# Kernel tuning notes

Hardware: AMD Instinct MI355X
Metric: run time of the kernel (lower is better)

The kernel has to match this reference:

```python
import jax, jax.numpy as jnp
import numpy as np

B = 8192
D = 512          # hidden_dim
OBS_EMB = 256
COMM = 128
N_ACT = 4
N_LAYERS = 2
D_INNER = 2 * D
D_STATE = 16
DT_RANK = D // 16  # 32
D_CONV = 4
EPS = 1e-5


def _xavier(k, shape):
    s = jnp.sqrt(2.0 / (shape[-2] + shape[-1]))
    return jax.random.normal(k, shape, jnp.float32) * s


def setup_inputs() -> dict:
    ks = jax.random.split(jax.random.key(0), 16)
    p = {}
    p['obs'] = jax.random.normal(ks[0], (B, 75), jnp.float32)
    p['comm_in'] = jax.random.normal(ks[1], (B, COMM), jnp.float32)
    # obs encoder: Conv2d(3->32, k=3, valid) + Linear(288->256)
    p['conv_w'] = jax.random.normal(ks[2], (32, 3, 3, 3), jnp.float32) * jnp.sqrt(2.0 / 27.0)
    p['conv_b'] = jnp.zeros((32,), jnp.float32)
    p['enc_w'] = _xavier(ks[3], (288, OBS_EMB))
    p['enc_b'] = jnp.zeros((OBS_EMB,), jnp.float32)
    p['proj_w'] = _xavier(ks[4], (OBS_EMB + COMM, D))
    p['proj_b'] = jnp.zeros((D,), jnp.float32)
    # Mamba stack params (stacked over layers)
    p['norm_w'] = jnp.ones((N_LAYERS, D), jnp.float32)
    p['in_proj_w'] = _xavier(ks[5], (N_LAYERS, D, 2 * D_INNER))
    p['conv1d_w'] = jax.random.normal(ks[6], (N_LAYERS, D_INNER, D_CONV), jnp.float32) / jnp.sqrt(D_CONV)
    p['conv1d_b'] = jnp.zeros((N_LAYERS, D_INNER), jnp.float32)
    p['x_proj_w'] = _xavier(ks[7], (N_LAYERS, D_INNER, DT_RANK + 2 * D_STATE))
    p['dt_proj_w'] = _xavier(ks[8], (N_LAYERS, DT_RANK, D_INNER))
    p['dt_proj_b'] = jnp.full((N_LAYERS, D_INNER), jnp.log(jnp.expm1(0.01)), jnp.float32)  # dt ~ 0.01
    p['A_log'] = jnp.log(jnp.broadcast_to(jnp.arange(1, D_STATE + 1, dtype=jnp.float32), (N_LAYERS, D_INNER, D_STATE)))
    p['D_param'] = jnp.ones((N_LAYERS, D_INNER), jnp.float32)
    p['out_proj_w'] = _xavier(ks[9], (N_LAYERS, D_INNER, D))
    p['final_norm_w'] = jnp.ones((D,), jnp.float32)
    # output heads
    p['act_w'] = _xavier(ks[10], (D, N_ACT)); p['act_b'] = jnp.zeros((N_ACT,), jnp.float32)
    p['comm_w'] = _xavier(ks[11], (D, COMM)); p['comm_b'] = jnp.zeros((COMM,), jnp.float32)
    p['val_w'] = _xavier(ks[12], (D, 1)); p['val_b'] = jnp.zeros((1,), jnp.float32)
    return p


def _rmsnorm(x, w):
    return x * jax.lax.rsqrt(jnp.mean(x * x, axis=-1, keepdims=True) + EPS) * w


def _mamba_block(u, Wi, cw, cb, Wx, Wdt, bdt, Alog, Dp, Wo):
    # u: (B, L, D) -> (B, L, D)
    Bsz, L, _ = u.shape
    d_inner = Dp.shape[0]
    x, z = jnp.split(u @ Wi, 2, axis=-1)                       # (B,L,di) each
    # causal depthwise conv1d over L
    xt = jnp.pad(jnp.swapaxes(x, 1, 2), ((0, 0), (0, 0), (D_CONV - 1, 0)))
    xc = jax.lax.conv_general_dilated(xt, cw[:, None, :], (1,), 'VALID',
                                      feature_group_count=d_inner,
                                      dimension_numbers=('NCH', 'OIH', 'NCH'))
    x = jax.nn.silu(jnp.swapaxes(xc, 1, 2) + cb)
    x_dbl = x @ Wx                                              # (B,L,dt_rank+2*ns)
    dt = jax.nn.softplus(x_dbl[..., :DT_RANK] @ Wdt + bdt)      # (B,L,di)
    Bm = x_dbl[..., DT_RANK:DT_RANK + D_STATE]                  # (B,L,ns)
    Cm = x_dbl[..., DT_RANK + D_STATE:]                         # (B,L,ns)
    A = -jnp.exp(Alog)                                          # (di,ns)
    dA = jnp.exp(dt[..., None] * A)                             # (B,L,di,ns)
    dBx = dt[..., None] * Bm[:, :, None, :] * x[..., None]      # (B,L,di,ns)

    def step(h, inp):
        dA_t, dBx_t, C_t = inp
        h = dA_t * h + dBx_t
        return h, jnp.einsum('bds,bs->bd', h, C_t)

    h0 = jnp.zeros((Bsz, d_inner, D_STATE), u.dtype)
    _, ys = jax.lax.scan(step, h0, (jnp.swapaxes(dA, 0, 1), jnp.swapaxes(dBx, 0, 1), jnp.swapaxes(Cm, 0, 1)))
    y = jnp.swapaxes(ys, 0, 1) + x * Dp
    return (y * jax.nn.silu(z)) @ Wo


def reference(obs, comm_in, conv_w, conv_b, enc_w, enc_b, proj_w, proj_b,
              norm_w, in_proj_w, conv1d_w, conv1d_b, x_proj_w, dt_proj_w, dt_proj_b,
              A_log, D_param, out_proj_w, final_norm_w,
              act_w, act_b, comm_w, comm_b, val_w, val_b):
    Bsz = obs.shape[0]
    v = obs.reshape(Bsz, 3, 5, 5)
    v = jax.lax.conv_general_dilated(v, conv_w, (1, 1), 'VALID',
                                     dimension_numbers=('NCHW', 'OIHW', 'NCHW'))
    v = jax.nn.relu(v + conv_b[None, :, None, None]).reshape(Bsz, -1)   # (B,288)
    emb = jax.nn.relu(v @ enc_w + enc_b)                                 # (B,256)
    x = jax.nn.relu(jnp.concatenate([emb, comm_in], axis=-1) @ proj_w + proj_b)  # (B,512)
    h = x[:, None, :]                                                    # (B, L=1, D)
    for i in range(norm_w.shape[0]):
        h = h + _mamba_block(_rmsnorm(h, norm_w[i]), in_proj_w[i], conv1d_w[i],
                             conv1d_b[i], x_proj_w[i], dt_proj_w[i], dt_proj_b[i],
                             A_log[i], D_param[i], out_proj_w[i])
    h = _rmsnorm(h, final_norm_w)[:, 0, :]
    action_logits = h @ act_w + act_b
    comm_out = jnp.tanh(h @ comm_w + comm_b)
    value = h @ val_w + val_b
    return action_logits, comm_out, value
```

## Files before the change

### kernel.cpp

```cpp
#include <hip/hip_runtime.h>
#include <math.h>


typedef __bf16 bf16x8 __attribute__((ext_vector_type(8)));
typedef float f32x4 __attribute__((ext_vector_type(4)));
typedef short short8 __attribute__((ext_vector_type(8)));

__device__ __forceinline__ float siluf(float v){ return v / (1.f + __expf(-v)); }
__device__ __forceinline__ float spfast(float v){ return v > 15.f ? v : __logf(1.f + __expf(v)); }
__device__ __forceinline__ float b2f(unsigned short u){ return __uint_as_float(((unsigned)u)<<16); }
__device__ __forceinline__ unsigned short f2b(float f){
  unsigned u = __float_as_uint(f);
  return (unsigned short)((u + 0x7fffu + ((u>>16)&1u)) >> 16);
}
__device__ __forceinline__ void g2l16(const void* g, void* l){
  __builtin_amdgcn_global_load_lds((const __attribute__((address_space(1))) unsigned int*)g,
                                   (__attribute__((address_space(3))) unsigned int*)l, 16, 0, 0);
}

__global__ __launch_bounds__(256) void k_wt_all(
    const float* __restrict__ in_proj_w, const float* __restrict__ out_proj_w,
    const float* __restrict__ x_proj_w,  const float* __restrict__ dt_proj_w,
    const float* __restrict__ enc_w,     const float* __restrict__ proj_w,
    const float* __restrict__ act_w, const float* __restrict__ comm_w, const float* __restrict__ val_w,
    const float* __restrict__ obs, const float* __restrict__ comm_in,
    const float* __restrict__ conv_w, const float* __restrict__ conv_b,
    unsigned short* __restrict__ wi_t, unsigned short* __restrict__ wo_t,
    unsigned short* __restrict__ wx_t, unsigned short* __restrict__ wdt_t,
    unsigned short* __restrict__ we_t, unsigned short* __restrict__ wp_t,
    unsigned short* __restrict__ wh_t,
    unsigned short* __restrict__ v, unsigned short* __restrict__ cat)
{
  int b = blockIdx.x;
  const int t = threadIdx.x;

  if (b >= 3792) {
    __shared__ float s_obs[8][76];
    const int r0 = (b - 3792) * 8;
    for (int i = t; i < 8*75; i += 256) s_obs[i/75][i%75] = obs[(size_t)(r0 + i/75)*75 + i%75];
    __syncthreads();
    for (int i = t; i < 8*288; i += 256) {
      int r = i / 288, o = i % 288;
      int c = o / 9, ij = o % 9, oi = ij/3, oj = ij%3;
      float acc = conv_b[c];
      #pragma unroll
      for (int ic=0; ic<3; ic++)
        #pragma unroll
        for (int ki=0; ki<3; ki++)
          #pragma unroll
          for (int kj=0; kj<3; kj++)
            acc = fmaf(s_obs[r][ic*25 + (oi+ki)*5 + (oj+kj)], conv_w[((c*3+ic)*3+ki)*3+kj], acc);
      v[(size_t)(r0+r)*320 + o] = f2b(fmaxf(acc, 0.f));
    }
    v[(size_t)(r0 + (t>>5))*320 + 288 + (t&31)] = 0;
    for (int i = t; i < 8*128; i += 256) {
      int r = i >> 7, c = i & 127;
      cat[(size_t)(r0+r)*384 + 256 + c] = f2b(comm_in[(size_t)(r0+r)*128 + c]);
    }
    return;
  }
  if (b >= 3536) {
    const int n = b - 3536;
    for (int k = t; k < 512; k += 256) {
      float v2;
      if (n < 4)         v2 = act_w[k*4 + n];
      else if (n < 132)  v2 = comm_w[k*128 + (n-4)];
      else if (n == 132) v2 = val_w[k];
      else               v2 = 0.f;
      wh_t[(size_t)n*512 + k] = f2b(v2);
    }
    return;
  }
  const float* Wsrc; unsigned short* Wdst; int Kd, Nd, KP, nkb;
  if (b < 2048) {
    const int L = b >> 10; b &= 1023;
    Wsrc = in_proj_w + (size_t)L*512*2048; Wdst = wi_t + (size_t)L*2048*512;
    Kd = 512; Nd = 2048; KP = 512; nkb = 16;
  } else if (b < 3072) {
    b -= 2048; const int L = b >> 9; b &= 511;
    Wsrc = out_proj_w + (size_t)L*1024*512; Wdst = wo_t + (size_t)L*512*1024;
    Kd = 1024; Nd = 512; KP = 1024; nkb = 32;
  } else if (b < 3200) {
    b -= 3072; const int L = b >> 6; b &= 63;
    Wsrc = x_proj_w + (size_t)L*1024*64; Wdst = wx_t + (size_t)L*64*1024;
    Kd = 1024; Nd = 64; KP = 1024; nkb = 32;
  } else if (b < 3264) {
    b -= 3200; const int L = b >> 5; b &= 31;
    Wsrc = dt_proj_w + (size_t)L*32*1024; Wdst = wdt_t + (size_t)L*1024*32;
    Kd = 32; Nd = 1024; KP = 32; nkb = 1;
  } else if (b < 3344) {
    b -= 3264; Wsrc = enc_w; Wdst = we_t; Kd = 288; Nd = 256; KP = 320; nkb = 10;
  } else {
    b -= 3344; Wsrc = proj_w; Wdst = wp_t; Kd = 384; Nd = 512; KP = 384; nkb = 12;
  }
  __shared__ float s[32][33];
  const int kb = (b % nkb)*32, nb = (b / nkb)*32;
  const int c = t & 31, r = t >> 5;
  #pragma unroll
  for (int i=0;i<32;i+=8) {
    const int k = kb + r + i;
    s[r+i][c] = (k < Kd) ? Wsrc[(size_t)k*Nd + nb + c] : 0.f;
  }
  __syncthreads();
  #pragma unroll
  for (int i=0;i<32;i+=8) Wdst[(size_t)(nb+r+i)*KP + kb + c] = f2b(s[c][r+i]);
}

__global__ __launch_bounds__(256) void k_rms(const float* __restrict__ h,
                                             const float* __restrict__ nw,
                                             unsigned short* __restrict__ u)
{
  const int l = threadIdx.x & 63;
  const size_t row = (size_t)blockIdx.x*4 + (threadIdx.x>>6);
  const float4* hp = (const float4*)(h + row*512) + l*2;
  float4 v0 = hp[0], v1 = hp[1];
  float ss = v0.x*v0.x+v0.y*v0.y+v0.z*v0.z+v0.w*v0.w
           + v1.x*v1.x+v1.y*v1.y+v1.z*v1.z+v1.w*v1.w;
  #pragma unroll
  for (int m=32;m;m>>=1) ss += __shfl_xor(ss, m, 64);
  const float sc = rsqrtf(ss*(1.f/512.f) + 1e-5f);
  const float4* np = (const float4*)nw + l*2;
  float4 w0 = np[0], w1 = np[1];
  short8 o;
  o[0]=(short)f2b(v0.x*sc*w0.x); o[1]=(short)f2b(v0.y*sc*w0.y);
  o[2]=(short)f2b(v0.z*sc*w0.z); o[3]=(short)f2b(v0.w*sc*w0.w);
  o[4]=(short)f2b(v1.x*sc*w1.x); o[5]=(short)f2b(v1.y*sc*w1.y);
  o[6]=(short)f2b(v1.z*sc*w1.z); o[7]=(short)f2b(v1.w*sc*w1.w);
  *(short8*)(u + row*512 + l*8) = o;
}

template<int K, int NB>
__device__ __forceinline__ void gemmT(const unsigned short* __restrict__ A,
                                      const unsigned short* __restrict__ Bt,
                                      int r0, int c0,
                                      unsigned short* sA, unsigned short* sB,
                                      f32x4 (&acc)[4][NB/32])
{
  constexpr int NF = NB/32;
  const int tid = threadIdx.x;
  const int l = tid & 63;
  const int wr = (tid>>7)&1, wc = (tid>>6)&1;
  const int rowA = tid>>3, kc8 = (tid&7)*8;
  const unsigned short* gA = A  + (size_t)(r0+rowA)*K + kc8;
  const unsigned short* gB = Bt + (size_t)(c0+rowA)*K + kc8;
  const int aOff = (wr*64 + (l&15))*64 + ((l>>4)*8);
  const int bOff = (wc*(NB/2) + (l&15))*64 + ((l>>4)*8);
  for (int kt=0; kt<K; kt+=64) {
    #pragma unroll
    for (int it=0; it<4; ++it) g2l16(gA + (size_t)(it*32)*K + kt, sA + ((it*256+tid)*8));
    #pragma unroll
    for (int it=0; it<NB/32; ++it) g2l16(gB + (size_t)(it*32)*K + kt, sB + ((it*256+tid)*8));
    __syncthreads();
    #pragma unroll
    for (int ks=0; ks<64; ks+=32) {
      bf16x8 af[4], bfm[NF];
      #pragma unroll
      for (int m=0;m<4;m++) af[m]  = *(const bf16x8*)(sA + (m*16)*64 + aOff + ks);
      #pragma unroll
      for (int n=0;n<NF;n++) bfm[n] = *(const bf16x8*)(sB + (n*16)*64 + bOff + ks);
      #pragma unroll
      for (int m=0;m<4;m++)
        #pragma unroll
        for (int n=0;n<NF;n++)
          acc[m][n] = __builtin_amdgcn_mfma_f32_16x16x32_bf16(af[m], bfm[n], acc[m][n], 0, 0, 0);
    }
    __syncthreads();
  }
}

__global__ __launch_bounds__(512) void k_gemm_inproj(
    const unsigned short* __restrict__ A, const unsigned short* __restrict__ Bt,
    const float* __restrict__ cw, const float* __restrict__ cb,
    unsigned short* __restrict__ xs, unsigned short* __restrict__ zs)
{
  __shared__ unsigned short sA[256*64], sB[128*64];
  f32x4 acc[4][4];
  #pragma unroll
  for (int m=0;m<4;m++)
    #pragma unroll
    for (int n=0;n<4;n++) acc[m][n] = (f32x4){0.f,0.f,0.f,0.f};
  const int tid = threadIdx.x, l = tid & 63;
  const int w = tid >> 6, wr = w >> 1, wc = w & 1;
  const int r0 = blockIdx.x*256, c0 = blockIdx.y*128;
  const int rowA = tid>>3, kc8 = (tid&7)*8;
  const unsigned short* gA = A  + (size_t)(r0+rowA)*512 + kc8;
  const unsigned short* gB = Bt + (size_t)(c0+rowA)*512 + kc8;
  const int aOff = (wr*64 + (l&15))*64 + ((l>>4)*8);
  const int bOff = (wc*64 + (l&15))*64 + ((l>>4)*8);
  for (int kt=0; kt<512; kt+=64) {
    #pragma unroll
    for (int it=0; it<4; ++it) g2l16(gA + (size_t)(it*64)*512 + kt, sA + ((it*512+tid)*8));
    #pragma unroll
    for (int it=0; it<2; ++it) g2l16(gB + (size_t)(it*64)*512 + kt, sB + ((it*512+tid)*8));
    __syncthreads();
    #pragma unroll
    for (int ks=0; ks<64; ks+=32) {
      bf16x8 af[4], bfm[4];
      #pragma unroll
      for (int m=0;m<4;m++) af[m]  = *(const bf16x8*)(sA + (m*16)*64 + aOff + ks);
      #pragma unroll
      for (int n=0;n<4;n++) bfm[n] = *(const bf16x8*)(sB + (n*16)*64 + bOff + ks);
      #pragma unroll
      for (int m=0;m<4;m++)
        #pragma unroll
        for (int n=0;n<4;n++)
          acc[m][n] = __builtin_amdgcn_mfma_f32_16x16x32_bf16(af[m], bfm[n], acc[m][n], 0, 0, 0);
    }
    __syncthreads();
  }
  const int colB = c0 + wc*64 + (l&15);
  const int rowB = r0 + wr*64 + ((l>>4)*4);
  if (c0 < 1024) {
    #pragma unroll
    for (int n=0;n<4;n++){
      const int col = colB + n*16;
      const float cw3 = cw[col*4+3], cbv = cb[col];
      #pragma unroll
      for (int m=0;m<4;m++)
        #pragma unroll
        for (int j=0;j<4;j++){
          const int row = rowB + m*16 + j;
          xs[(size_t)row*1024 + col] = f2b(siluf(fmaf(acc[m][n][j], cw3, cbv)));
        }
    }
  } else {
    #pragma unroll
    for (int n=0;n<4;n++){
      const int col = colB + n*16 - 1024;
      #pragma unroll
      for (int m=0;m<4;m++)
        #pragma unroll
        for (int j=0;j<4;j++){
          const int row = rowB + m*16 + j;
          zs[(size_t)row*1024 + col] = f2b(siluf(acc[m][n][j]));
        }
    }
  }
}

__global__ __launch_bounds__(256) void k_gemm_outproj(
    const unsigned short* __restrict__ A, const unsigned short* __restrict__ Bt,
    float* __restrict__ h)
{
  __shared__ unsigned short sA[128*64], sB[64*64];
  f32x4 acc[4][2];
  #pragma unroll
  for (int m=0;m<4;m++)
    #pragma unroll
    for (int n=0;n<2;n++) acc[m][n] = (f32x4){0.f,0.f,0.f,0.f};
  const int r0 = blockIdx.x*128, c0 = blockIdx.y*64;
  gemmT<1024,64>(A, Bt, r0, c0, sA, sB, acc);

  const int tid = threadIdx.x, l = tid & 63;
  const int wr = (tid>>7)&1, wc = (tid>>6)&1;
  const int colB = c0 + wc*32 + (l&15);
  const int rowB = r0 + wr*64 + ((l>>4)*4);
  #pragma unroll
  for (int n=0;n<2;n++){
    const int col = colB + n*16;
    #pragma unroll
    for (int m=0;m<4;m++)
      #pragma unroll
      for (int j=0;j<4;j++){
        const int row = rowB + m*16 + j;
        h[(size_t)row*512 + col] += acc[m][n][j];
      }
  }
}

__global__ __launch_bounds__(256) void k_gemm_enc(
    const unsigned short* __restrict__ A, const unsigned short* __restrict__ Bt,
    const float* __restrict__ bias, unsigned short* __restrict__ cat)
{
  __shared__ unsigned short sA[128*64], sB[64*64];
  f32x4 acc[4][2];
  #pragma unroll
  for (int m=0;m<4;m++)
    #pragma unroll
    for (int n=0;n<2;n++) acc[m][n] = (f32x4){0.f,0.f,0.f,0.f};
  const int r0 = blockIdx.x*128, c0 = blockIdx.y*64;
  gemmT<320,64>(A, Bt, r0, c0, sA, sB, acc);

  const int tid = threadIdx.x, l = tid & 63;
  const int wr = (tid>>7)&1, wc = (tid>>6)&1;
  const int colB = c0 + wc*32 + (l&15);
  const int rowB = r0 + wr*64 + ((l>>4)*4);
  #pragma unroll
  for (int n=0;n<2;n++){
    const int col = colB + n*16;
    const float bv = bias[col];
    #pragma unroll
    for (int m=0;m<4;m++)
      #pragma unroll
      for (int j=0;j<4;j++){
        const size_t row = rowB + m*16 + j;
        cat[row*384 + col] = f2b(fmaxf(acc[m][n][j] + bv, 0.f));
      }
  }
}

__global__ __launch_bounds__(256) void k_gemm_proj(
    const unsigned short* __restrict__ A, const unsigned short* __restrict__ Bt,
    const float* __restrict__ bias, float* __restrict__ h)
{
  __shared__ unsigned short sA[128*64], sB[64*64];
  f32x4 acc[4][2];
  #pragma unroll
  for (int m=0;m<4;m++)
    #pragma unroll
    for (int n=0;n<2;n++) acc[m][n] = (f32x4){0.f,0.f,0.f,0.f};
  const int r0 = blockIdx.x*128, c0 = blockIdx.y*64;
  gemmT<384,64>(A, Bt, r0, c0, sA, sB, acc);

  const int tid = threadIdx.x, l = tid & 63;
  const int wr = (tid>>7)&1, wc = (tid>>6)&1;
  const int colB = c0 + wc*32 + (l&15);
  const int rowB = r0 + wr*64 + ((l>>4)*4);
  #pragma unroll
  for (int n=0;n<2;n++){
    const int col = colB + n*16;
    const float bv = bias[col];
    #pragma unroll
    for (int m=0;m<4;m++)
      #pragma unroll
      for (int j=0;j<4;j++){
        const size_t row = rowB + m*16 + j;
        h[row*512 + col] = fmaxf(acc[m][n][j] + bv, 0.f);
      }
  }
}

__global__ __launch_bounds__(256) void k_gemm_heads(
    const unsigned short* __restrict__ A, const unsigned short* __restrict__ Bt,
    const float* __restrict__ act_b, const float* __restrict__ comm_b,
    const float* __restrict__ val_b, float* __restrict__ out)
{
  __shared__ unsigned short sA[128*64], sB[64*64];
  f32x4 acc[4][2];
  #pragma unroll
  for (int m=0;m<4;m++)
    #pragma unroll
    for (int n=0;n<2;n++) acc[m][n] = (f32x4){0.f,0.f,0.f,0.f};
  const int r0 = blockIdx.x*128, c0 = blockIdx.y*64;
  gemmT<512,64>(A, Bt, r0, c0, sA, sB, acc);

  const int tid = threadIdx.x, l = tid & 63;
  const int wr = (tid>>7)&1, wc = (tid>>6)&1;
  const int colB = c0 + wc*32 + (l&15);
  const int rowB = r0 + wr*64 + ((l>>4)*4);
  #pragma unroll
  for (int n=0;n<2;n++){
    const int col = colB + n*16;
    if (col > 132) continue;
    #pragma unroll
    for (int m=0;m<4;m++)
      #pragma unroll
      for (int j=0;j<4;j++){
        const size_t row = rowB + m*16 + j;
        float v = acc[m][n][j];
        if (col < 4)        out[row*4 + col] = v + act_b[col];
        else if (col < 132) out[32768 + row*128 + (col-4)] = tanhf(v + comm_b[col-4]);
        else                out[1081344 + row] = v + val_b[0];
      }
  }
}

__global__ __launch_bounds__(256) void k_ssm_f(
    unsigned short* __restrict__ xs, const unsigned short* __restrict__ zs,
    const unsigned short* __restrict__ Wx_t, const unsigned short* __restrict__ Wdt_t,
    const float* __restrict__ bdt, const float* __restrict__ Dp)
{
  __shared__ unsigned short sX[32*1024];
  __shared__ unsigned short sB[64*128];
  __shared__ float s_dbl[32][64];
  __shared__ unsigned short sDt[32*32];
  __shared__ float s_bc[32];
  const int tid = threadIdx.x, l = tid & 63, w = tid >> 6;
  const int r0 = blockIdx.x * 32;

  #pragma unroll
  for (int it=0; it<16; ++it) {
    const int idx = it*256 + tid;
    g2l16(xs + (size_t)(r0 + (idx>>7))*1024 + (idx&127)*8, sX + idx*8);
  }

  f32x4 acc0 = (f32x4){0.f,0.f,0.f,0.f}, acc1 = (f32x4){0.f,0.f,0.f,0.f};
  for (int kt = 0; kt < 1024; kt += 128) {
    #pragma unroll
    for (int it=0; it<4; ++it) {
      const int idx = it*256 + tid;
      g2l16(Wx_t + (size_t)(idx>>4)*1024 + (idx&15)*8 + kt, sB + idx*8);
    }
    __syncthreads();
    #pragma unroll
    for (int ks=0; ks<128; ks+=32) {
      bf16x8 a0 = *(const bf16x8*)(sX + ((l&15))*1024    + (l>>4)*8 + kt + ks);
      bf16x8 a1 = *(const bf16x8*)(sX + (16+(l&15))*1024 + (l>>4)*8 + kt + ks);
      bf16x8 bf = *(const bf16x8*)(sB + (w*16+(l&15))*128 + (l>>4)*8 + ks);
      acc0 = __builtin_amdgcn_mfma_f32_16x16x32_bf16(a0, bf, acc0, 0, 0, 0);
      acc1 = __builtin_amdgcn_mfma_f32_16x16x32_bf16(a1, bf, acc1, 0, 0, 0);
    }
    __syncthreads();
  }
  #pragma unroll
  for (int j=0;j<4;j++) {
    s_dbl[(l>>4)*4 + j]     [w*16 + (l&15)] = acc0[j];
    s_dbl[16 + (l>>4)*4 + j][w*16 + (l&15)] = acc1[j];
  }
  __syncthreads();
  if (tid < 32) {
    float a = 0.f;
    #pragma unroll
    for (int s=0;s<16;s++) a = fmaf(s_dbl[tid][32+s], s_dbl[tid][48+s], a);
    s_bc[tid] = a;
  }
  {
    const int r = tid >> 3, c4 = (tid & 7)*4;
    sDt[r*32 + c4]   = f2b(s_dbl[r][c4]);
    sDt[r*32 + c4+1] = f2b(s_dbl[r][c4+1]);
    sDt[r*32 + c4+2] = f2b(s_dbl[r][c4+2]);
    sDt[r*32 + c4+3] = f2b(s_dbl[r][c4+3]);
  }
  __syncthreads();

  bf16x8 af0 = *(const bf16x8*)(sDt + ((l&15))*32    + (l>>4)*8);
  bf16x8 af1 = *(const bf16x8*)(sDt + (16+(l&15))*32 + (l>>4)*8);
  for (int c = 0; c < 4; ++c) {
    const int cc = c*256;
    #pragma unroll
    for (int it=0; it<4; ++it) {
      const int idx = it*256 + tid;
      g2l16(Wdt_t + (size_t)(cc + (idx>>2))*32 + (idx&3)*8, sB + idx*8);
    }
    __syncthreads();
    f32x4 a2[2][4];
    #pragma unroll
    for (int n=0;n<4;n++){
      bf16x8 bn = *(const bf16x8*)(sB + (w*64 + n*16 + (l&15))*32 + (l>>4)*8);
      a2[0][n] = __builtin_amdgcn_mfma_f32_16x16x32_bf16(af0, bn, (f32x4){0.f,0.f,0.f,0.f}, 0, 0, 0);
      a2[1][n] = __builtin_amdgcn_mfma_f32_16x16x32_bf16(af1, bn, (f32x4){0.f,0.f,0.f,0.f}, 0, 0, 0);
    }
    #pragma unroll
    for (int n=0;n<4;n++){
      const int col = cc + w*64 + n*16 + (l&15);
      const float bj = bdt[col], dpj = Dp[col];
      #pragma unroll
      for (int m=0;m<2;m++){
        #pragma unroll
        for (int j=0;j<4;j++){
          const int rloc = m*16 + (l>>4)*4 + j;
          const size_t row = r0 + rloc;
          const float dtv = spfast(a2[m][n][j] + bj);
          const float f = fmaf(dtv, s_bc[rloc], dpj);
          const float x = b2f(sX[rloc*1024 + col]);
          const float z = b2f(zs[row*1024 + col]);
          xs[row*1024 + col] = f2b(x * f * z);
        }
      }
    }
    __syncthreads();
  }
}

extern "C" void kernel_launch(void* const* d_in, const int* in_sizes, int n_in,
                              void* d_out, int out_size, void* d_ws, size_t ws_size,
                              hipStream_t stream) {
  const float* obs       = (const float*)d_in[0];
  const float* comm_in   = (const float*)d_in[1];
  const float* conv_w    = (const float*)d_in[2];
  const float* conv_b    = (const float*)d_in[3];
  const float* enc_w     = (const float*)d_in[4];
  const float* enc_b     = (const float*)d_in[5];
  const float* proj_w    = (const float*)d_in[6];
  const float* proj_b    = (const float*)d_in[7];
  const float* norm_w    = (const float*)d_in[8];
  const float* in_proj_w = (const float*)d_in[9];
  const float* conv1d_w  = (const float*)d_in[10];
  const float* conv1d_b  = (const float*)d_in[11];
  const float* x_proj_w  = (const float*)d_in[12];
  const float* dt_proj_w = (const float*)d_in[13];
  const float* dt_proj_b = (const float*)d_in[14];
  const float* D_param   = (const float*)d_in[16];
  const float* out_proj_w= (const float*)d_in[17];
  const float* final_nw  = (const float*)d_in[18];
  const float* act_w     = (const float*)d_in[19];
  const float* act_b     = (const float*)d_in[20];
  const float* comm_w    = (const float*)d_in[21];
  const float* comm_b    = (const float*)d_in[22];
  const float* val_w     = (const float*)d_in[23];
  const float* val_b     = (const float*)d_in[24];
  float* out = (float*)d_out;

  char* W = (char*)d_ws;
  float* h             = (float*)W;
  unsigned short* u_b  = (unsigned short*)(W + (16u<<20));
  unsigned short* xs_b = (unsigned short*)(W + (24u<<20));
  unsigned short* zs_b = (unsigned short*)(W + (40u<<20));
  unsigned short* wi_t = (unsigned short*)(W + (56u<<20));
  unsigned short* wo_t = (unsigned short*)(W + (60u<<20));
  unsigned short* wx_t = (unsigned short*)(W + (64u<<20));
  unsigned short* wdt_t= (unsigned short*)(W + (64u<<20) + (256u<<10));
  unsigned short* wh_t = (unsigned short*)(W + (65u<<20));
  unsigned short* we_t = (unsigned short*)(W + (65u<<20) + (512u<<10));
  unsigned short* wp_t = (unsigned short*)(W + (66u<<20));

  unsigned short* v_b   = xs_b;
  unsigned short* cat_b = zs_b;

  k_wt_all<<<4816,256,0,stream>>>(in_proj_w, out_proj_w, x_proj_w, dt_proj_w,
                                  enc_w, proj_w, act_w, comm_w, val_w,
                                  obs, comm_in, conv_w, conv_b,
                                  wi_t, wo_t, wx_t, wdt_t, we_t, wp_t, wh_t,
                                  v_b, cat_b);

  k_gemm_enc<<<dim3(64,4),256,0,stream>>>(v_b, we_t, enc_b, cat_b);
  k_gemm_proj<<<dim3(64,8),256,0,stream>>>(cat_b, wp_t, proj_b, h);

  for (int L=0; L<2; L++) {
    k_rms<<<2048,256,0,stream>>>(h, norm_w + L*512, u_b);
    k_gemm_inproj<<<dim3(32,16),512,0,stream>>>(u_b, wi_t + (size_t)L*2048*512,
                                                conv1d_w + L*1024*4, conv1d_b + L*1024, xs_b, zs_b);
    k_ssm_f<<<256,256,0,stream>>>(xs_b, zs_b, wx_t + (size_t)L*64*1024,
                                  wdt_t + (size_t)L*1024*32,
                                  dt_proj_b + L*1024, D_param + L*1024);
    k_gemm_outproj<<<dim3(64,8),256,0,stream>>>(xs_b, wo_t + (size_t)L*512*1024, h);
  }
  k_rms<<<2048,256,0,stream>>>(h, final_nw, u_b);
  k_gemm_heads<<<dim3(64,4),256,0,stream>>>(u_b, wh_t, act_b, comm_b, val_b, out);
}
```

Measured before the change: 256.2 us.

## Double-buffer LDS tiles in GEMMs and SSM kernel, retile in_proj GEMM

The shared GEMM helper and the SSM kernel's x_proj and dt_proj loops now use two LDS buffers. The next K-tile is fetched with global_load_lds while the current one feeds the MFMAs, removing one barrier per iteration and hiding some load latency. The in_proj GEMM moves from a 256x128 tile with 512 threads to a 128x128 tile with 256 threads so it can reuse the pipelined helper. LDS use per block doubles, which can lower occupancy, and overlap depends on the compiler not forcing an early vmcnt wait before the LDS reads.

```diff
diff --git a/kernel.cpp b/kernel.cpp
--- a/kernel.cpp
+++ b/kernel.cpp
@@ -137,6 +137,7 @@
                                       f32x4 (&acc)[4][NB/32])
 {
   constexpr int NF = NB/32;
+  constexpr int ABUF = 128*64, BBUF = NB*64;
   const int tid = threadIdx.x;
   const int l = tid & 63;
   const int wr = (tid>>7)&1, wc = (tid>>6)&1;
@@ -145,19 +146,30 @@
   const unsigned short* gB = Bt + (size_t)(c0+rowA)*K + kc8;
   const int aOff = (wr*64 + (l&15))*64 + ((l>>4)*8);
   const int bOff = (wc*(NB/2) + (l&15))*64 + ((l>>4)*8);
+
+  auto stage = [&](int kt, int buf) {
+    #pragma unroll
+    for (int it=0; it<4; ++it)
+      g2l16(gA + (size_t)(it*32)*K + kt, sA + buf*ABUF + (it*256+tid)*8);
+    #pragma unroll
+    for (int it=0; it<NF; ++it)
+      g2l16(gB + (size_t)(it*32)*K + kt, sB + buf*BBUF + (it*256+tid)*8);
+  };
+
+  stage(0, 0);
+  __syncthreads();
+  int cur = 0;
   for (int kt=0; kt<K; kt+=64) {
-    #pragma unroll
-    for (int it=0; it<4; ++it) g2l16(gA + (size_t)(it*32)*K + kt, sA + ((it*256+tid)*8));
-    #pragma unroll
-    for (int it=0; it<NB/32; ++it) g2l16(gB + (size_t)(it*32)*K + kt, sB + ((it*256+tid)*8));
-    __syncthreads();
+    if (kt + 64 < K) stage(kt + 64, cur ^ 1);
+    const unsigned short* pA = sA + cur*ABUF;
+    const unsigned short* pB = sB + cur*BBUF;
     #pragma unroll
     for (int ks=0; ks<64; ks+=32) {
       bf16x8 af[4], bfm[NF];
       #pragma unroll
-      for (int m=0;m<4;m++) af[m]  = *(const bf16x8*)(sA + (m*16)*64 + aOff + ks);
-      #pragma unroll
-      for (int n=0;n<NF;n++) bfm[n] = *(const bf16x8*)(sB + (n*16)*64 + bOff + ks);
+      for (int m=0;m<4;m++) af[m]  = *(const bf16x8*)(pA + (m*16)*64 + aOff + ks);
+      #pragma unroll
+      for (int n=0;n<NF;n++) bfm[n] = *(const bf16x8*)(pB + (n*16)*64 + bOff + ks);
       #pragma unroll
       for (int m=0;m<4;m++)
         #pragma unroll
@@ -165,49 +177,26 @@
           acc[m][n] = __builtin_amdgcn_mfma_f32_16x16x32_bf16(af[m], bfm[n], acc[m][n], 0, 0, 0);
     }
     __syncthreads();
-  }
-}
-
-__global__ __launch_bounds__(512) void k_gemm_inproj(
+    cur ^= 1;
+  }
+}
+
+__global__ __launch_bounds__(256) void k_gemm_inproj(
     const unsigned short* __restrict__ A, const unsigned short* __restrict__ Bt,
     const float* __restrict__ cw, const float* __restrict__ cb,
     unsigned short* __restrict__ xs, unsigned short* __restrict__ zs)
 {
-  __shared__ unsigned short sA[256*64], sB[128*64];
+  __shared__ unsigned short sA[2*128*64], sB[2*128*64];
   f32x4 acc[4][4];
   #pragma unroll
   for (int m=0;m<4;m++)
     #pragma unroll
     for (int n=0;n<4;n++) acc[m][n] = (f32x4){0.f,0.f,0.f,0.f};
+  const int r0 = blockIdx.x*128, c0 = blockIdx.y*128;
+  gemmT<512,128>(A, Bt, r0, c0, sA, sB, acc);
+
   const int tid = threadIdx.x, l = tid & 63;
-  const int w = tid >> 6, wr = w >> 1, wc = w & 1;
-  const int r0 = blockIdx.x*256, c0 = blockIdx.y*128;
-  const int rowA = tid>>3, kc8 = (tid&7)*8;
-  const unsigned short* gA = A  + (size_t)(r0+rowA)*512 + kc8;
-  const unsigned short* gB = Bt + (size_t)(c0+rowA)*512 + kc8;
-  const int aOff = (wr*64 + (l&15))*64 + ((l>>4)*8);
-  const int bOff = (wc*64 + (l&15))*64 + ((l>>4)*8);
-  for (int kt=0; kt<512; kt+=64) {
-    #pragma unroll
-    for (int it=0; it<4; ++it) g2l16(gA + (size_t)(it*64)*512 + kt, sA + ((it*512+tid)*8));
-    #pragma unroll
-    for (int it=0; it<2; ++it) g2l16(gB + (size_t)(it*64)*512 + kt, sB + ((it*512+tid)*8));
-    __syncthreads();
-    #pragma unroll
-    for (int ks=0; ks<64; ks+=32) {
-      bf16x8 af[4], bfm[4];
-      #pragma unroll
-      for (int m=0;m<4;m++) af[m]  = *(const bf16x8*)(sA + (m*16)*64 + aOff + ks);
-      #pragma unroll
-      for (int n=0;n<4;n++) bfm[n] = *(const bf16x8*)(sB + (n*16)*64 + bOff + ks);
-      #pragma unroll
-      for (int m=0;m<4;m++)
-        #pragma unroll
-        for (int n=0;n<4;n++)
-          acc[m][n] = __builtin_amdgcn_mfma_f32_16x16x32_bf16(af[m], bfm[n], acc[m][n], 0, 0, 0);
-    }
-    __syncthreads();
-  }
+  const int wr = (tid>>7)&1, wc = (tid>>6)&1;
   const int colB = c0 + wc*64 + (l&15);
   const int rowB = r0 + wr*64 + ((l>>4)*4);
   if (c0 < 1024) {
@@ -242,7 +231,7 @@
     const unsigned short* __restrict__ A, const unsigned short* __restrict__ Bt,
     float* __restrict__ h)
 {
-  __shared__ unsigned short sA[128*64], sB[64*64];
+  __shared__ unsigned short sA[2*128*64], sB[2*64*64];
   f32x4 acc[4][2];
   #pragma unroll
   for (int m=0;m<4;m++)
@@ -272,7 +261,7 @@
     const unsigned short* __restrict__ A, const unsigned short* __restrict__ Bt,
     const float* __restrict__ bias, unsigned short* __restrict__ cat)
 {
-  __shared__ unsigned short sA[128*64], sB[64*64];
+  __shared__ unsigned short sA[2*128*64], sB[2*64*64];
   f32x4 acc[4][2];
   #pragma unroll
   for (int m=0;m<4;m++)
@@ -303,7 +292,7 @@
     const unsigned short* __restrict__ A, const unsigned short* __restrict__ Bt,
     const float* __restrict__ bias, float* __restrict__ h)
 {
-  __shared__ unsigned short sA[128*64], sB[64*64];
+  __shared__ unsigned short sA[2*128*64], sB[2*64*64];
   f32x4 acc[4][2];
   #pragma unroll
   for (int m=0;m<4;m++)
@@ -335,7 +324,7 @@
     const float* __restrict__ act_b, const float* __restrict__ comm_b,
     const float* __restrict__ val_b, float* __restrict__ out)
 {
-  __shared__ unsigned short sA[128*64], sB[64*64];
+  __shared__ unsigned short sA[2*128*64], sB[2*64*64];
   f32x4 acc[4][2];
   #pragma unroll
   for (int m=0;m<4;m++)
@@ -371,37 +360,57 @@
     const float* __restrict__ bdt, const float* __restrict__ Dp)
 {
   __shared__ unsigned short sX[32*1024];
-  __shared__ unsigned short sB[64*128];
+  __shared__ unsigned short sB[2*64*128];
   __shared__ float s_dbl[32][64];
   __shared__ unsigned short sDt[32*32];
   __shared__ float s_bc[32];
+  constexpr int BB = 64*128;
   const int tid = threadIdx.x, l = tid & 63, w = tid >> 6;
   const int r0 = blockIdx.x * 32;
+
+  auto stageWx = [&](int kt, int buf) {
+    #pragma unroll
+    for (int it=0; it<4; ++it) {
+      const int idx = it*256 + tid;
+      g2l16(Wx_t + (size_t)(idx>>4)*1024 + (idx&15)*8 + kt, sB + buf*BB + idx*8);
+    }
+  };
 
   #pragma unroll
   for (int it=0; it<16; ++it) {
     const int idx = it*256 + tid;
     g2l16(xs + (size_t)(r0 + (idx>>7))*1024 + (idx&127)*8, sX + idx*8);
   }
+  stageWx(0, 0);
+  __syncthreads();
 
   f32x4 acc0 = (f32x4){0.f,0.f,0.f,0.f}, acc1 = (f32x4){0.f,0.f,0.f,0.f};
+  int cur = 0;
   for (int kt = 0; kt < 1024; kt += 128) {
-    #pragma unroll
-    for (int it=0; it<4; ++it) {
-      const int idx = it*256 + tid;
-      g2l16(Wx_t + (size_t)(idx>>4)*1024 + (idx&15)*8 + kt, sB + idx*8);
-    }
-    __syncthreads();
+    if (kt + 128 < 1024) stageWx(kt + 128, cur ^ 1);
+    const unsigned short* pB = sB + cur*BB;
     #pragma unroll
     for (int ks=0; ks<128; ks+=32) {
       bf16x8 a0 = *(const bf16x8*)(sX + ((l&15))*1024    + (l>>4)*8 + kt + ks);
       bf16x8 a1 = *(const bf16x8*)(sX + (16+(l&15))*1024 + (l>>4)*8 + kt + ks);
-      bf16x8 bf = *(const bf16x8*)(sB + (w*16+(l&15))*128 + (l>>4)*8 + ks);
+      bf16x8 bf = *(const bf16x8*)(pB + (w*16+(l&15))*128 + (l>>4)*8 + ks);
       acc0 = __builtin_amdgcn_mfma_f32_16x16x32_bf16(a0, bf, acc0, 0, 0, 0);
       acc1 = __builtin_amdgcn_mfma_f32_16x16x32_bf16(a1, bf, acc1, 0, 0, 0);
     }
     __syncthreads();
-  }
+    cur ^= 1;
+  }
+
+  auto stageWdt = [&](int c, int buf) {
+    const int cc = c*256;
+    #pragma unroll
+    for (int it=0; it<4; ++it) {
+      const int idx = it*256 + tid;
+      g2l16(Wdt_t + (size_t)(cc + (idx>>2))*32 + (idx&3)*8, sB + buf*BB + idx*8);
+    }
+  };
+  stageWdt(0, 0);
+
   #pragma unroll
   for (int j=0;j<4;j++) {
     s_dbl[(l>>4)*4 + j]     [w*16 + (l&15)] = acc0[j];
@@ -426,20 +435,16 @@
   bf16x8 af0 = *(const bf16x8*)(sDt + ((l&15))*32    + (l>>4)*8);
   bf16x8 af1 = *(const bf16x8*)(sDt + (16+(l&15))*32 + (l>>4)*8);
   for (int c = 0; c < 4; ++c) {
-    const int cc = c*256;
-    #pragma unroll
-    for (int it=0; it<4; ++it) {
-      const int idx = it*256 + tid;
-      g2l16(Wdt_t + (size_t)(cc + (idx>>2))*32 + (idx&3)*8, sB + idx*8);
-    }
-    __syncthreads();
+    if (c + 1 < 4) stageWdt(c + 1, (c + 1) & 1);
+    const unsigned short* pB = sB + (c & 1)*BB;
     f32x4 a2[2][4];
     #pragma unroll
     for (int n=0;n<4;n++){
-      bf16x8 bn = *(const bf16x8*)(sB + (w*64 + n*16 + (l&15))*32 + (l>>4)*8);
+      bf16x8 bn = *(const bf16x8*)(pB + (w*64 + n*16 + (l&15))*32 + (l>>4)*8);
       a2[0][n] = __builtin_amdgcn_mfma_f32_16x16x32_bf16(af0, bn, (f32x4){0.f,0.f,0.f,0.f}, 0, 0, 0);
       a2[1][n] = __builtin_amdgcn_mfma_f32_16x16x32_bf16(af1, bn, (f32x4){0.f,0.f,0.f,0.f}, 0, 0, 0);
     }
+    const int cc = c*256;
     #pragma unroll
     for (int n=0;n<4;n++){
       const int col = cc + w*64 + n*16 + (l&15);
@@ -518,7 +523,7 @@
 
   for (int L=0; L<2; L++) {
     k_rms<<<2048,256,0,stream>>>(h, norm_w + L*512, u_b);
-    k_gemm_inproj<<<dim3(32,16),512,0,stream>>>(u_b, wi_t + (size_t)L*2048*512,
+    k_gemm_inproj<<<dim3(64,16),256,0,stream>>>(u_b, wi_t + (size_t)L*2048*512,
                                                 conv1d_w + L*1024*4, conv1d_b + L*1024, xs_b, zs_b);
     k_ssm_f<<<256,256,0,stream>>>(xs_b, zs_b, wx_t + (size_t)L*64*1024,
                                   wdt_t + (size_t)L*1024*32,
```

New measurement: 235.2 us. 8.2% less time.
